# Kernel tuning notes

Measured on AMD Instinct MI355X. Metric: run time of the kernel, lower is better.

Reference implementation:

```python
import jax, jax.numpy as jnp
import numpy as np

DIM = 128
N_VAR = 100000
N_CON = 100000
N_NODES = 200000
N_EDGES = 640000


def setup_inputs() -> dict:
    key = jax.random.key(0)
    ks = jax.random.split(key, 25)
    d = DIM
    u = lambda k, s: jax.random.uniform(k, s, jnp.float32, -0.1, 0.1)
    inp = {
        "var_node_features": jax.random.normal(ks[0], (N_VAR, 2), jnp.float32),
        "con_node_features": jax.random.normal(ks[1], (N_CON, 2), jnp.float32),
        "node_types": jax.random.randint(ks[2], (N_NODES,), 0, 2),
        "assoc_var": jnp.arange(N_VAR),
        "assoc_con": N_VAR + jnp.arange(N_CON),
        "edge_index": jax.random.randint(ks[3], (2, N_EDGES), 0, N_NODES),
        "edge_types": jax.random.randint(ks[4], (N_EDGES,), 0, 2),
        "edge_features": jax.random.normal(ks[5], (N_EDGES, 1), jnp.float32),
        "var_w1": u(ks[6], (2, d)), "var_b1": u(ks[7], (d,)),
        "var_w2": u(ks[8], (d, d)), "var_b2": u(ks[9], (d,)),
        "con_w1": u(ks[10], (2, d)), "con_b1": u(ks[11], (d,)),
        "con_w2": u(ks[12], (d, d)), "con_b2": u(ks[13], (d,)),
    }
    for i, k0 in zip((1, 2, 3), (14, 17, 20)):
        inp[f"basis{i}"] = u(ks[k0], (1, d, d))      # num_bases=1
        inp[f"att{i}"] = u(ks[k0 + 1], (2, 1))       # num_relations=2
        inp[f"root{i}"] = u(ks[k0 + 2], (d, d))
        inp[f"bias{i}"] = jnp.zeros((d,), jnp.float32)
    inp["fc1_w"] = u(ks[23], (4 * d, d))
    inp["fc1_b"] = jnp.zeros((d,), jnp.float32)
    inp["fc4_w"] = u(ks[24], (d, 1))
    inp["fc4_b"] = jnp.zeros((1,), jnp.float32)
    return inp


def rgcn(x, src, dst, etype, basis, att, root, bias):
    # basis: [1, d, d], att: [2, 1] -> per-relation weights [2, d, d]
    d = x.shape[-1]
    w = (att @ basis.reshape(basis.shape[0], -1)).reshape(2, d, d)
    xj = x[src]  # [E, d] gather
    # only 2 relations: two GEMMs + select (avoids [E,d,d] materialization)
    msg = jnp.where((etype == 0)[:, None], xj @ w[0], xj @ w[1])
    s = jax.ops.segment_sum(msg, dst, num_segments=N_NODES)
    cnt = jax.ops.segment_sum(jnp.ones((dst.shape[0],), x.dtype), dst, num_segments=N_NODES)
    agg = s / jnp.maximum(cnt, 1.0)[:, None]  # mean aggregation
    return agg + x @ root + bias


def reference(var_node_features, con_node_features, node_types, assoc_var, assoc_con,
              edge_index, edge_types, edge_features,
              var_w1, var_b1, var_w2, var_b2,
              con_w1, con_b1, con_w2, con_b2,
              basis1, att1, root1, bias1,
              basis2, att2, root2, bias2,
              basis3, att3, root3, bias3,
              fc1_w, fc1_b, fc4_w, fc4_b):
    n = jnp.maximum(var_node_features @ var_w1 + var_b1, 0.0) @ var_w2 + var_b2
    e = jnp.maximum(con_node_features @ con_w1 + con_b1, 0.0) @ con_w2 + con_b2
    x = jnp.zeros((node_types.shape[0], n.shape[-1]), n.dtype)
    x = x.at[assoc_var].set(n).at[assoc_con].set(e)
    src, dst = edge_index[0], edge_index[1]
    x1 = jax.nn.relu(rgcn(x, src, dst, edge_types, basis1, att1, root1, bias1))
    x2 = jax.nn.relu(rgcn(x1, src, dst, edge_types, basis2, att2, root2, bias2))
    x3 = jax.nn.relu(rgcn(x2, src, dst, edge_types, basis3, att3, root3, bias3))
    h = jnp.concatenate([x, x1, x2, x3], axis=-1)[assoc_var]  # [n_var, 4d]
    h = jax.nn.relu(h @ fc1_w + fc1_b)
    # dropout p=0.5 is identity in eval mode
    return (h @ fc4_w + fc4_b)[:, 0]
```

## Files before the change

### kernel.cpp

```cpp
#include <hip/hip_runtime.h>
#include <hip/hip_bf16.h>

#define D 128
#define NV 100000
#define NC 100000
#define NN 200000
#define NE 640000

typedef __attribute__((ext_vector_type(4))) float f32x4;
typedef __attribute__((ext_vector_type(8))) short bf16x8;

static __device__ __forceinline__ unsigned short f2b(float f) {
    __hip_bfloat16 h = __float2bfloat16(f);
    union { __hip_bfloat16 h; unsigned short u; } c; c.h = h; return c.u;
}
static __device__ __forceinline__ float b2f(unsigned short b) {
    union { unsigned int u; float f; } c; c.u = ((unsigned int)b) << 16; return c.f;
}

template<bool RELU>
static __device__ __forceinline__ void split8v(const float f[8], bf16x8& ah, bf16x8& al)
{
    union { unsigned short s[8]; bf16x8 v; } ph, pl;
    #pragma unroll
    for (int j = 0; j < 8; ++j) {
        float x = RELU ? fmaxf(f[j], 0.f) : f[j];
        ph.s[j] = f2b(x);
        pl.s[j] = f2b(x - b2f(ph.s[j]));
    }
    ah = ph.v; al = pl.v;
}

union H8 { _Float16 h[8]; uint4 u; };
union H4 { _Float16 h[4]; uint2 u; };

struct PrepArgs { const float* src[12]; };

__global__ __launch_bounds__(256, 1) void prep_kernel(PrepArgs a, unsigned short* wt)
{
    const float* W = a.src[blockIdx.y];
    unsigned short* hi = wt + (size_t)blockIdx.y * 32768;
    unsigned short* lo = hi + 16384;
    const int o = blockIdx.x * 1024 + threadIdx.x * 4;
    const int slice = o >> 10;
    const int n     = (o >> 3) & 127;
    const int j0    = o & 7;
    union { unsigned short s[4]; unsigned long long u; } ph, pl;
    #pragma unroll
    for (int i = 0; i < 4; ++i) {
        const int k = slice * 8 + j0 + i;
        const float w = W[k * 128 + n];
        ph.s[i] = f2b(w);
        pl.s[i] = f2b(w - b2f(ph.s[i]));
    }
    *(unsigned long long*)&hi[o] = ph.u;
    *(unsigned long long*)&lo[o] = pl.u;
}

static __device__ __forceinline__ const bf16x8* wfrag(const unsigned short* wt,
                                                      int ks, int lg, int n)
{
    return (const bf16x8*)(wt + (((ks * 4 + lg) * 128) + n) * 8);
}

static __device__ __forceinline__ char* haddr(char* base, int row, int byteoff)
{
    return base + row * 256 + (byteoff ^ ((row & 7) << 4));
}

template<int AMODE, bool RELU_A>
static __device__ __forceinline__ void stage16(
    const void* A, const _Float16* agg, const float* w1, const float* b1,
    int M, int tt, int srow, int skf, int ob0, int ob1, char* hb, char* lb)
{
    int grow = tt * 32 + srow; if (grow >= M) grow = M - 1;
    float f[16];
    if (AMODE == 2) {
        const float* fr = (const float*)A + (size_t)grow * 2;
        const float f0 = fr[0], f1 = fr[1];
        #pragma unroll
        for (int q = 0; q < 4; ++q) {
            const float4 wa = *(const float4*)(w1 + skf + q * 4);
            const float4 wb = *(const float4*)(w1 + 128 + skf + q * 4);
            const float4 bb = *(const float4*)(b1 + skf + q * 4);
            f[q * 4 + 0] = fmaxf(fmaf(f0, wa.x, fmaf(f1, wb.x, bb.x)), 0.f);
            f[q * 4 + 1] = fmaxf(fmaf(f0, wa.y, fmaf(f1, wb.y, bb.y)), 0.f);
            f[q * 4 + 2] = fmaxf(fmaf(f0, wa.z, fmaf(f1, wb.z, bb.z)), 0.f);
            f[q * 4 + 3] = fmaxf(fmaf(f0, wa.w, fmaf(f1, wb.w, bb.w)), 0.f);
        }
    } else {
        const _Float16* ap = (const _Float16*)A + (size_t)grow * D + skf;
        H8 a0, a1; a0.u = ((const uint4*)ap)[0]; a1.u = ((const uint4*)ap)[1];
        #pragma unroll
        for (int j = 0; j < 8; ++j) { f[j] = (float)a0.h[j]; f[8 + j] = (float)a1.h[j]; }
        if (AMODE == 1) {
            const _Float16* gp = agg + (size_t)grow * D + skf;
            H8 g0, g1; g0.u = ((const uint4*)gp)[0]; g1.u = ((const uint4*)gp)[1];
            #pragma unroll
            for (int j = 0; j < 8; ++j) { f[j] += (float)g0.h[j]; f[8 + j] += (float)g1.h[j]; }
        }
    }
    bf16x8 h0, l0, h1, l1;
    split8v<RELU_A>(&f[0], h0, l0);
    split8v<RELU_A>(&f[8], h1, l1);
    char* hbr = hb + srow * 256;
    char* lbr = lb + srow * 256;
    *(bf16x8*)(hbr + ob0) = h0; *(bf16x8*)(hbr + ob1) = h1;
    *(bf16x8*)(lbr + ob0) = l0; *(bf16x8*)(lbr + ob1) = l1;
}

template<int AMODE, bool RELU_A, bool ADD_C>
__global__ __launch_bounds__(256, 4) void gemm5(
    const void* A, const _Float16* __restrict__ agg,
    const float* __restrict__ w1, const float* __restrict__ b1, int M,
    const unsigned short* __restrict__ wt, const float* __restrict__ bias,
    _Float16* Cout)
{
    __shared__ unsigned short Hs[2][2][32 * 128];
    const int tid  = threadIdx.x;
    const int lane = tid & 63, wv = tid >> 6;
    const int li   = lane & 15, lg = lane >> 4;
    const int colbase = wv * 32;

    bf16x8 bh[4][2], bl[4][2];
    #pragma unroll
    for (int ks = 0; ks < 4; ++ks)
        #pragma unroll
        for (int nf = 0; nf < 2; ++nf) {
            const int n = colbase + nf * 16 + li;
            bh[ks][nf] = *wfrag(wt,         ks, lg, n);
            bl[ks][nf] = *wfrag(wt + 16384, ks, lg, n);
        }

    const int ntiles = (M + 31) / 32;
    const int G = gridDim.x;
    const int t0 = blockIdx.x;
    if (t0 >= ntiles) return;

    const int srow = tid >> 3;
    const int skf  = (tid & 7) * 16;
    const int sw   = (srow & 7) << 4;
    const int ob0  = (skf * 2) ^ sw;
    const int ob1  = (skf * 2 + 16) ^ sw;

    stage16<AMODE, RELU_A>(A, agg, w1, b1, M, t0, srow, skf, ob0, ob1,
                           (char*)&Hs[0][0][0], (char*)&Hs[0][1][0]);
    __syncthreads();

    int cur = 0;
    for (int t = t0; t < ntiles; t += G) {
        const int tn = t + G;

        char* hb = (char*)&Hs[cur][0][0];
        char* lb = (char*)&Hs[cur][1][0];
        f32x4 acc[2][2];
        #pragma unroll
        for (int ms = 0; ms < 2; ++ms)
            #pragma unroll
            for (int nf = 0; nf < 2; ++nf) acc[ms][nf] = (f32x4){0.f, 0.f, 0.f, 0.f};
        #pragma unroll
        for (int ks = 0; ks < 4; ++ks) {
            const int kb = ks * 64 + lg * 16;
            bf16x8 ah[2], al[2];
            #pragma unroll
            for (int ms = 0; ms < 2; ++ms) {
                const int row = ms * 16 + li;
                ah[ms] = *(const bf16x8*)haddr(hb, row, kb);
                al[ms] = *(const bf16x8*)haddr(lb, row, kb);
            }
            #pragma unroll
            for (int nf = 0; nf < 2; ++nf)
                #pragma unroll
                for (int ms = 0; ms < 2; ++ms) {
                    acc[ms][nf] = __builtin_amdgcn_mfma_f32_16x16x32_bf16(bh[ks][nf], ah[ms], acc[ms][nf], 0, 0, 0);
                    acc[ms][nf] = __builtin_amdgcn_mfma_f32_16x16x32_bf16(bh[ks][nf], al[ms], acc[ms][nf], 0, 0, 0);
                    acc[ms][nf] = __builtin_amdgcn_mfma_f32_16x16x32_bf16(bl[ks][nf], ah[ms], acc[ms][nf], 0, 0, 0);
                }
        }

        #pragma unroll
        for (int ms = 0; ms < 2; ++ms) {
            const int grow = t * 32 + ms * 16 + li;
            if (grow < M) {
                _Float16* crow = Cout + (size_t)grow * D;
                #pragma unroll
                for (int nf = 0; nf < 2; ++nf) {
                    const int c0 = colbase + nf * 16 + lg * 4;
                    float v[4];
                    #pragma unroll
                    for (int r = 0; r < 4; ++r) v[r] = acc[ms][nf][r];
                    if (bias) {
                        const float4 b = *(const float4*)(bias + c0);
                        v[0] += b.x; v[1] += b.y; v[2] += b.z; v[3] += b.w;
                    }
                    H4 pk;
                    if (ADD_C) {
                        H4 rd; rd.u = *(const uint2*)(crow + c0);
                        #pragma unroll
                        for (int r = 0; r < 4; ++r) v[r] += (float)rd.h[r];
                    }
                    #pragma unroll
                    for (int r = 0; r < 4; ++r) pk.h[r] = (_Float16)v[r];
                    *(uint2*)(crow + c0) = pk.u;
                }
            }
        }

        if (tn < ntiles)
            stage16<AMODE, RELU_A>(A, agg, w1, b1, M, tn, srow, skf, ob0, ob1,
                                   (char*)&Hs[cur ^ 1][0][0], (char*)&Hs[cur ^ 1][1][0]);
        __syncthreads();
        cur ^= 1;
    }
}

template<bool RELU_A, bool HASAGG>
__global__ __launch_bounds__(512, 4) void layer5(
    _Float16* x, const _Float16* __restrict__ agg, int M, int Mroot,
    const unsigned short* __restrict__ wtb, const unsigned short* __restrict__ wtr,
    const float* __restrict__ bias, unsigned short* __restrict__ y)
{
    __shared__ unsigned short Hs[2][2][32 * 128];
    const int tid  = threadIdx.x;
    const int lane = tid & 63, wv = tid >> 6;
    const int li   = lane & 15, lg = lane >> 4;
    const int isroot  = wv >> 2;
    const int colbase = (wv & 3) * 32;
    const unsigned short* wsel = isroot ? wtr : wtb;

    bf16x8 bh[4][2], bl[4][2];
    #pragma unroll
    for (int ks = 0; ks < 4; ++ks)
        #pragma unroll
        for (int nf = 0; nf < 2; ++nf) {
            const int n = colbase + nf * 16 + li;
            bh[ks][nf] = *wfrag(wsel,         ks, lg, n);
            bl[ks][nf] = *wfrag(wsel + 16384, ks, lg, n);
        }
    float4 bv[2] = {{0,0,0,0},{0,0,0,0}};
    if (isroot) {
        bv[0] = *(const float4*)(bias + colbase + 0  + lg * 4);
        bv[1] = *(const float4*)(bias + colbase + 16 + lg * 4);
    }

    const int ntiles = (M + 31) / 32;
    const int G = gridDim.x;
    const int t0 = blockIdx.x;
    if (t0 >= ntiles) return;

    const int srow = tid >> 4;
    const int skf  = (tid & 15) * 8;
    const int sw   = (srow & 7) << 4;
    const int ob0  = (skf * 2) ^ sw;

    #define STAGE_L(TT, BUF)                                                     \
    {                                                                            \
        int grow = (TT) * 32 + srow; if (grow >= M) grow = M - 1;                \
        const _Float16* ap = x + (size_t)grow * D + skf;                         \
        H8 a0; a0.u = *(const uint4*)ap;                                         \
        float f[8];                                                              \
        _Pragma("unroll")                                                        \
        for (int j = 0; j < 8; ++j) f[j] = (float)a0.h[j];                       \
        if (HASAGG) {                                                            \
            H8 g0; g0.u = *(const uint4*)(agg + (size_t)grow * D + skf);         \
            _Pragma("unroll")                                                    \
            for (int j = 0; j < 8; ++j) f[j] += (float)g0.h[j];                  \
        }                                                                        \
        bf16x8 h0, l0;                                                           \
        split8v<RELU_A>(f, h0, l0);                                             \
        *(bf16x8*)((char*)&Hs[BUF][0][0] + srow * 256 + ob0) = h0;               \
        *(bf16x8*)((char*)&Hs[BUF][1][0] + srow * 256 + ob0) = l0;               \
    }

    STAGE_L(t0, 0);
    __syncthreads();

    int cur = 0;
    for (int t = t0; t < ntiles; t += G) {
        const int tn = t + G;

        char* hb = (char*)&Hs[cur][0][0];
        char* lb = (char*)&Hs[cur][1][0];
        f32x4 acc[2][2];
        #pragma unroll
        for (int ms = 0; ms < 2; ++ms)
            #pragma unroll
            for (int nf = 0; nf < 2; ++nf) acc[ms][nf] = (f32x4){0.f, 0.f, 0.f, 0.f};
        #pragma unroll
        for (int ks = 0; ks < 4; ++ks) {
            const int kb = ks * 64 + lg * 16;
            bf16x8 ah[2], al[2];
            #pragma unroll
            for (int ms = 0; ms < 2; ++ms) {
                const int row = ms * 16 + li;
                ah[ms] = *(const bf16x8*)haddr(hb, row, kb);
                al[ms] = *(const bf16x8*)haddr(lb, row, kb);
            }
            #pragma unroll
            for (int nf = 0; nf < 2; ++nf)
                #pragma unroll
                for (int ms = 0; ms < 2; ++ms) {
                    acc[ms][nf] = __builtin_amdgcn_mfma_f32_16x16x32_bf16(bh[ks][nf], ah[ms], acc[ms][nf], 0, 0, 0);
                    acc[ms][nf] = __builtin_amdgcn_mfma_f32_16x16x32_bf16(bh[ks][nf], al[ms], acc[ms][nf], 0, 0, 0);
                    acc[ms][nf] = __builtin_amdgcn_mfma_f32_16x16x32_bf16(bl[ks][nf], ah[ms], acc[ms][nf], 0, 0, 0);
                }
        }

        #pragma unroll
        for (int ms = 0; ms < 2; ++ms) {
            const int grow = t * 32 + ms * 16 + li;
            if (!isroot) {
                if (grow < M) {
                    unsigned short* yrow = y + (size_t)grow * D;
                    #pragma unroll
                    for (int nf = 0; nf < 2; ++nf) {
                        const int c0 = colbase + nf * 16 + lg * 4;
                        union { unsigned short s[4]; uint2 v; } pk;
                        #pragma unroll
                        for (int r = 0; r < 4; ++r) pk.s[r] = f2b(acc[ms][nf][r]);
                        *(uint2*)(yrow + c0) = pk.v;
                    }
                }
            } else {
                if (grow < Mroot) {
                    _Float16* xrow = x + (size_t)grow * D;
                    #pragma unroll
                    for (int nf = 0; nf < 2; ++nf) {
                        const int c0 = colbase + nf * 16 + lg * 4;
                        const float bb[4] = {bv[nf].x, bv[nf].y, bv[nf].z, bv[nf].w};
                        H4 pk;
                        #pragma unroll
                        for (int r = 0; r < 4; ++r) pk.h[r] = (_Float16)(acc[ms][nf][r] + bb[r]);
                        *(uint2*)(xrow + c0) = pk.u;
                    }
                }
            }
        }

        if (tn < ntiles) STAGE_L(tn, cur ^ 1);
        __syncthreads();
        cur ^= 1;
    }
    #undef STAGE_L
}

__global__ void hist_kernel(const int* __restrict__ dst, int* __restrict__ deg, int ne)
{
    int g = blockIdx.x * blockDim.x + threadIdx.x;
    if (g < ne) atomicAdd(&deg[dst[g]], 1);
}

__global__ __launch_bounds__(256, 1) void scan_blk(int* __restrict__ buf,
                                                   int* __restrict__ sums, int n)
{
    __shared__ int part[256];
    const int tid  = threadIdx.x;
    const int base = blockIdx.x * 1024 + tid * 4;
    int v0 = (base + 0 < n) ? buf[base + 0] : 0;
    int v1 = (base + 1 < n) ? buf[base + 1] : 0;
    int v2 = (base + 2 < n) ? buf[base + 2] : 0;
    int v3 = (base + 3 < n) ? buf[base + 3] : 0;
    const int t0 = v0, t1 = t0 + v1, t2 = t1 + v2, t3 = t2 + v3;
    part[tid] = t3;
    __syncthreads();
    #pragma unroll
    for (int off = 1; off < 256; off <<= 1) {
        int x = part[tid];
        if (tid >= off) x += part[tid - off];
        __syncthreads();
        part[tid] = x;
        __syncthreads();
    }
    if (tid == 255) sums[blockIdx.x] = part[255];
    const int excl = tid ? part[tid - 1] : 0;
    if (base + 0 < n) buf[base + 0] = excl;
    if (base + 1 < n) buf[base + 1] = excl + t0;
    if (base + 2 < n) buf[base + 2] = excl + t1;
    if (base + 3 < n) buf[base + 3] = excl + t2;
}

__global__ __launch_bounds__(256, 1) void scan_top(int* __restrict__ sums, int nb)
{
    __shared__ int part[256];
    const int tid = threadIdx.x;
    part[tid] = (tid < nb) ? sums[tid] : 0;
    __syncthreads();
    #pragma unroll
    for (int off = 1; off < 256; off <<= 1) {
        int x = part[tid];
        if (tid >= off) x += part[tid - off];
        __syncthreads();
        part[tid] = x;
        __syncthreads();
    }
    if (tid < nb) sums[tid] = tid ? part[tid - 1] : 0;
}

__global__ void scan_add(int* __restrict__ buf, const int* __restrict__ sums, int n)
{
    int i = blockIdx.x * blockDim.x + threadIdx.x;
    if (i < n) buf[i] += sums[i >> 10];
}

__global__ void fill_kernel(const int* __restrict__ src, const int* __restrict__ dst,
                            const int* __restrict__ etype,
                            int* __restrict__ cursor, int* __restrict__ edges, int ne)
{
    int e = blockIdx.x * blockDim.x + threadIdx.x;
    if (e < ne) {
        const int pos = atomicAdd(&cursor[dst[e]], 1);
        edges[pos] = (src[e] << 1) | (etype[e] & 1);
    }
}

__global__ __launch_bounds__(256, 2) void gather_agg(
    const int* __restrict__ cursor, const int* __restrict__ edges,
    const float* __restrict__ att, const unsigned short* __restrict__ y,
    _Float16* __restrict__ agg, int nn)
{
    const int gid  = blockIdx.x * 256 + threadIdx.x;
    const int node = gid >> 4;
    const int l    = gid & 15;
    if (node >= nn) return;
    const int end   = cursor[node];
    const int start = node ? cursor[node - 1] : 0;
    const float a0 = att[0], a1 = att[1];
    float s0[8] = {0,0,0,0,0,0,0,0}, s1[8] = {0,0,0,0,0,0,0,0};
    int j = start;
    for (; j + 2 <= end; j += 2) {
        const int p0 = edges[j], p1 = edges[j + 1];
        const float w0 = (p0 & 1) ? a1 : a0;
        const float w1 = (p1 & 1) ? a1 : a0;
        const uint4 va = ((const uint4*)(y + ((size_t)(p0 >> 1)) * D))[l];
        const uint4 vb = ((const uint4*)(y + ((size_t)(p1 >> 1)) * D))[l];
        const unsigned int wa[4] = {va.x, va.y, va.z, va.w};
        const unsigned int wb[4] = {vb.x, vb.y, vb.z, vb.w};
        #pragma unroll
        for (int q = 0; q < 4; ++q) {
            s0[q * 2 + 0] = fmaf(w0, b2f((unsigned short)(wa[q] & 0xFFFF)), s0[q * 2 + 0]);
            s0[q * 2 + 1] = fmaf(w0, b2f((unsigned short)(wa[q] >> 16)),    s0[q * 2 + 1]);
            s1[q * 2 + 0] = fmaf(w1, b2f((unsigned short)(wb[q] & 0xFFFF)), s1[q * 2 + 0]);
            s1[q * 2 + 1] = fmaf(w1, b2f((unsigned short)(wb[q] >> 16)),    s1[q * 2 + 1]);
        }
    }
    if (j < end) {
        const int p0 = edges[j];
        const float w0 = (p0 & 1) ? a1 : a0;
        const uint4 va = ((const uint4*)(y + ((size_t)(p0 >> 1)) * D))[l];
        const unsigned int wa[4] = {va.x, va.y, va.z, va.w};
        #pragma unroll
        for (int q = 0; q < 4; ++q) {
            s0[q * 2 + 0] = fmaf(w0, b2f((unsigned short)(wa[q] & 0xFFFF)), s0[q * 2 + 0]);
            s0[q * 2 + 1] = fmaf(w0, b2f((unsigned short)(wa[q] >> 16)),    s0[q * 2 + 1]);
        }
    }
    const float inv = 1.0f / fmaxf((float)(end - start), 1.0f);
    H8 o;
    #pragma unroll
    for (int q = 0; q < 8; ++q) o.h[q] = (_Float16)((s0[q] + s1[q]) * inv);
    *(uint4*)(agg + (size_t)node * D + l * 8) = o.u;
}

__global__ void final_kernel(
    const _Float16* __restrict__ u, const float* __restrict__ fc1_b,
    const float* __restrict__ fc4_w, const float* __restrict__ fc4_b,
    float* __restrict__ out, int n)
{
    int gid = blockIdx.x * blockDim.x + threadIdx.x;
    int row = gid >> 5, lane = gid & 31;
    if (row >= n) return;
    H4 uv; uv.u = ((const uint2*)(u + (size_t)row * D))[lane];
    float4 b = ((const float4*)fc1_b)[lane];
    float4 w = ((const float4*)fc4_w)[lane];
    float s = fmaxf((float)uv.h[0] + b.x, 0.f) * w.x
            + fmaxf((float)uv.h[1] + b.y, 0.f) * w.y
            + fmaxf((float)uv.h[2] + b.z, 0.f) * w.z
            + fmaxf((float)uv.h[3] + b.w, 0.f) * w.w;
    #pragma unroll
    for (int off = 1; off < 32; off <<= 1) s += __shfl_xor(s, off);
    if (lane == 0) out[row] = s + fc4_b[0];
}

extern "C" void kernel_launch(void* const* d_in, const int* in_sizes, int n_in,
                              void* d_out, int out_size, void* d_ws, size_t ws_size,
                              hipStream_t stream)
{
    const float* varf      = (const float*)d_in[0];
    const float* conf      = (const float*)d_in[1];
    const int*   edge_src  = (const int*)d_in[5];
    const int*   edge_dst  = edge_src + NE;
    const int*   etype     = (const int*)d_in[6];
    const float* var_w1 = (const float*)d_in[8];
    const float* var_b1 = (const float*)d_in[9];
    const float* var_w2 = (const float*)d_in[10];
    const float* var_b2 = (const float*)d_in[11];
    const float* con_w1 = (const float*)d_in[12];
    const float* con_b1 = (const float*)d_in[13];
    const float* con_w2 = (const float*)d_in[14];
    const float* con_b2 = (const float*)d_in[15];
    const float* basisL[3] = {(const float*)d_in[16], (const float*)d_in[20], (const float*)d_in[24]};
    const float* attL[3]   = {(const float*)d_in[17], (const float*)d_in[21], (const float*)d_in[25]};
    const float* rootL[3]  = {(const float*)d_in[18], (const float*)d_in[22], (const float*)d_in[26]};
    const float* biasL[3]  = {(const float*)d_in[19], (const float*)d_in[23], (const float*)d_in[27]};
    const float* fc1_w = (const float*)d_in[28];
    const float* fc1_b = (const float*)d_in[29];
    const float* fc4_w = (const float*)d_in[30];
    const float* fc4_b = (const float*)d_in[31];

    const size_t XB  = (size_t)NN * D * 2;
    const size_t YB  = (size_t)NN * D * 2;
    const size_t AB  = (size_t)NN * D * 2;
    const size_t UB  = (size_t)NV * D * 2;
    const size_t CUR = (size_t)NN * 4;
    const size_t EDG = (size_t)NE * 4;
    const size_t SUM = 4096;
    const size_t WT  = (size_t)12 * 32768 * 2;
    const size_t need = XB + YB + AB + UB + CUR + EDG + SUM + WT;
    if (ws_size < need) {
        hipMemsetAsync(d_out, 0, (size_t)out_size * sizeof(float), stream);
        return;
    }
    char* p = (char*)d_ws;
    _Float16*       x      = (_Float16*)p;       p += XB;
    unsigned short* y      = (unsigned short*)p; p += YB;
    _Float16*       agg    = (_Float16*)p;       p += AB;
    _Float16*       u      = (_Float16*)p;       p += UB;
    int*            cursor = (int*)p;            p += CUR;
    int*            edges  = (int*)p;            p += EDG;
    int*            sums   = (int*)p;            p += SUM;
    unsigned short* wt     = (unsigned short*)p;

    PrepArgs pa;
    pa.src[0] = basisL[0]; pa.src[1] = basisL[1]; pa.src[2] = basisL[2];
    pa.src[3] = rootL[0];  pa.src[4] = rootL[1];  pa.src[5] = rootL[2];
    pa.src[6] = fc1_w;                 pa.src[7] = fc1_w + 128 * 128;
    pa.src[8] = fc1_w + 2 * 128 * 128; pa.src[9] = fc1_w + 3 * 128 * 128;
    pa.src[10] = var_w2;               pa.src[11] = con_w2;
    prep_kernel<<<dim3(16, 12), 256, 0, stream>>>(pa, wt);

    hipMemsetAsync(cursor, 0, CUR, stream);
    hist_kernel<<<(NE + 255) / 256, 256, 0, stream>>>(edge_dst, cursor, NE);
    const int nblk = (NN + 1023) / 1024;
    scan_blk<<<nblk, 256, 0, stream>>>(cursor, sums, NN);
    scan_top<<<1, 256, 0, stream>>>(sums, nblk);
    scan_add<<<(NN + 255) / 256, 256, 0, stream>>>(cursor, sums, NN);
    fill_kernel<<<(NE + 255) / 256, 256, 0, stream>>>(edge_src, edge_dst, etype,
                                                      cursor, edges, NE);

    const int GM = 1024;
    const int GL = 1024;

    gemm5<2, false, false><<<GM, 256, 0, stream>>>(
        varf, nullptr, var_w1, var_b1, NV, wt + (size_t)10 * 32768, var_b2, x);
    gemm5<2, false, false><<<GM, 256, 0, stream>>>(
        conf, nullptr, con_w1, con_b1, NC, wt + (size_t)11 * 32768, con_b2,
        x + (size_t)NV * D);

    gemm5<0, false, false><<<GM, 256, 0, stream>>>(
        x, nullptr, nullptr, nullptr, NV, wt + (size_t)6 * 32768, nullptr, u);

    for (int l = 0; l < 3; ++l) {
        const unsigned short* wb_ = wt + (size_t)l * 32768;
        const unsigned short* wr_ = wt + (size_t)(3 + l) * 32768;
        const int mroot = (l == 2) ? NV : NN;
        const int gn    = (l == 2) ? NV : NN;
        if (l == 0)
            layer5<false, false><<<GL, 512, 0, stream>>>(x, nullptr, NN, mroot, wb_, wr_, biasL[0], y);
        else
            layer5<true, true><<<GL, 512, 0, stream>>>(x, agg, NN, mroot, wb_, wr_, biasL[l], y);
        gather_agg<<<(gn * 16 + 255) / 256, 256, 0, stream>>>(
            cursor, edges, attL[l], y, agg, gn);
        gemm5<1, true, true><<<GM, 256, 0, stream>>>(
            x, agg, nullptr, nullptr, NV, wt + (size_t)(7 + l) * 32768, nullptr, u);
    }

    final_kernel<<<(NV * 32 + 255) / 256, 256, 0, stream>>>(
        u, fc1_b, fc4_w, fc4_b, (float*)d_out, NV);
}
```

Before: 442.0 us.

## Fuse fc1 partial GEMMs into layer kernels and prefetch next tile into registers

Each layer kernel gets a third group of four waves, 768 threads per block, that multiplies the staged activation tile by the matching fc1 weight slice and accumulates into u. This removes the separate fc1 GEMM passes that re-read x and agg. Only the last layer's fc1 slice keeps its own GEMM. Both GEMM kernels now load the next tile's global data into registers before the MFMA loop and write it to shared memory afterwards, so load latency overlaps compute. The changes add register pressure, drop occupancy bounds to 3 blocks, and cut the layer grid to 256 blocks, which may reduce parallelism.

New measurement: 411.9 us (median of 2 runs). 1.07x faster.

```diff
diff --git a/kernel.cpp b/kernel.cpp
--- a/kernel.cpp
+++ b/kernel.cpp
@@ -68,49 +68,27 @@
     return base + row * 256 + (byteoff ^ ((row & 7) << 4));
 }
 
-template<int AMODE, bool RELU_A>
-static __device__ __forceinline__ void stage16(
-    const void* A, const _Float16* agg, const float* w1, const float* b1,
-    int M, int tt, int srow, int skf, int ob0, int ob1, char* hb, char* lb)
-{
-    int grow = tt * 32 + srow; if (grow >= M) grow = M - 1;
-    float f[16];
-    if (AMODE == 2) {
-        const float* fr = (const float*)A + (size_t)grow * 2;
-        const float f0 = fr[0], f1 = fr[1];
-        #pragma unroll
-        for (int q = 0; q < 4; ++q) {
-            const float4 wa = *(const float4*)(w1 + skf + q * 4);
-            const float4 wb = *(const float4*)(w1 + 128 + skf + q * 4);
-            const float4 bb = *(const float4*)(b1 + skf + q * 4);
-            f[q * 4 + 0] = fmaxf(fmaf(f0, wa.x, fmaf(f1, wb.x, bb.x)), 0.f);
-            f[q * 4 + 1] = fmaxf(fmaf(f0, wa.y, fmaf(f1, wb.y, bb.y)), 0.f);
-            f[q * 4 + 2] = fmaxf(fmaf(f0, wa.z, fmaf(f1, wb.z, bb.z)), 0.f);
-            f[q * 4 + 3] = fmaxf(fmaf(f0, wa.w, fmaf(f1, wb.w, bb.w)), 0.f);
-        }
-    } else {
-        const _Float16* ap = (const _Float16*)A + (size_t)grow * D + skf;
-        H8 a0, a1; a0.u = ((const uint4*)ap)[0]; a1.u = ((const uint4*)ap)[1];
-        #pragma unroll
-        for (int j = 0; j < 8; ++j) { f[j] = (float)a0.h[j]; f[8 + j] = (float)a1.h[j]; }
-        if (AMODE == 1) {
-            const _Float16* gp = agg + (size_t)grow * D + skf;
-            H8 g0, g1; g0.u = ((const uint4*)gp)[0]; g1.u = ((const uint4*)gp)[1];
-            #pragma unroll
-            for (int j = 0; j < 8; ++j) { f[j] += (float)g0.h[j]; f[8 + j] += (float)g1.h[j]; }
-        }
-    }
-    bf16x8 h0, l0, h1, l1;
-    split8v<RELU_A>(&f[0], h0, l0);
-    split8v<RELU_A>(&f[8], h1, l1);
-    char* hbr = hb + srow * 256;
-    char* lbr = lb + srow * 256;
-    *(bf16x8*)(hbr + ob0) = h0; *(bf16x8*)(hbr + ob1) = h1;
-    *(bf16x8*)(lbr + ob0) = l0; *(bf16x8*)(lbr + ob1) = l1;
+template<bool RELU, bool HASAGG>
+static __device__ __forceinline__ void wsplit8(uint4 xv, uint4 gv,
+                                               char* hb, char* lb, int srow, int ob0)
+{
+    H8 a0; a0.u = xv;
+    float f[8];
+    #pragma unroll
+    for (int j = 0; j < 8; ++j) f[j] = (float)a0.h[j];
+    if (HASAGG) {
+        H8 g0; g0.u = gv;
+        #pragma unroll
+        for (int j = 0; j < 8; ++j) f[j] += (float)g0.h[j];
+    }
+    bf16x8 h0, l0;
+    split8v<RELU>(f, h0, l0);
+    *(bf16x8*)(hb + srow * 256 + ob0) = h0;
+    *(bf16x8*)(lb + srow * 256 + ob0) = l0;
 }
 
 template<int AMODE, bool RELU_A, bool ADD_C>
-__global__ __launch_bounds__(256, 4) void gemm5(
+__global__ __launch_bounds__(256, 4) void gemm6(
     const void* A, const _Float16* __restrict__ agg,
     const float* __restrict__ w1, const float* __restrict__ b1, int M,
     const unsigned short* __restrict__ wt, const float* __restrict__ bias,
@@ -143,13 +121,64 @@
     const int ob0  = (skf * 2) ^ sw;
     const int ob1  = (skf * 2 + 16) ^ sw;
 
-    stage16<AMODE, RELU_A>(A, agg, w1, b1, M, t0, srow, skf, ob0, ob1,
-                           (char*)&Hs[0][0][0], (char*)&Hs[0][1][0]);
+    #define LOADT(TT, XV0, XV1, GV0, GV1, FV)                                    \
+    {                                                                            \
+        int grow = (TT) * 32 + srow; if (grow >= M) grow = M - 1;                \
+        if (AMODE == 2) {                                                        \
+            FV = *(const float2*)((const float*)A + (size_t)grow * 2);           \
+        } else {                                                                 \
+            const uint4* ap = (const uint4*)((const _Float16*)A + (size_t)grow * D + skf); \
+            XV0 = ap[0]; XV1 = ap[1];                                            \
+            if (AMODE == 1) {                                                    \
+                const uint4* gp = (const uint4*)(agg + (size_t)grow * D + skf);  \
+                GV0 = gp[0]; GV1 = gp[1];                                        \
+            }                                                                    \
+        }                                                                        \
+    }
+    #define WRITET(BUF, XV0, XV1, GV0, GV1, FV)                                  \
+    {                                                                            \
+        char* hb_ = (char*)&Hs[BUF][0][0];                                       \
+        char* lb_ = (char*)&Hs[BUF][1][0];                                       \
+        if (AMODE == 2) {                                                        \
+            float f[16];                                                         \
+            const float f0 = FV.x, f1 = FV.y;                                    \
+            _Pragma("unroll")                                                    \
+            for (int q = 0; q < 4; ++q) {                                        \
+                const float4 wa = *(const float4*)(w1 + skf + q * 4);            \
+                const float4 wb = *(const float4*)(w1 + 128 + skf + q * 4);      \
+                const float4 bb = *(const float4*)(b1 + skf + q * 4);            \
+                f[q*4+0] = fmaxf(fmaf(f0, wa.x, fmaf(f1, wb.x, bb.x)), 0.f);     \
+                f[q*4+1] = fmaxf(fmaf(f0, wa.y, fmaf(f1, wb.y, bb.y)), 0.f);     \
+                f[q*4+2] = fmaxf(fmaf(f0, wa.z, fmaf(f1, wb.z, bb.z)), 0.f);     \
+                f[q*4+3] = fmaxf(fmaf(f0, wa.w, fmaf(f1, wb.w, bb.w)), 0.f);     \
+            }                                                                    \
+            bf16x8 h0, l0, h1, l1;                                               \
+            split8v<RELU_A>(&f[0], h0, l0);                                     \
+            split8v<RELU_A>(&f[8], h1, l1);                                     \
+            char* hbr = hb_ + srow * 256; char* lbr = lb_ + srow * 256;          \
+            *(bf16x8*)(hbr + ob0) = h0; *(bf16x8*)(hbr + ob1) = h1;              \
+            *(bf16x8*)(lbr + ob0) = l0; *(bf16x8*)(lbr + ob1) = l1;              \
+        } else {                                                                 \
+            wsplit8<RELU_A, AMODE == 1>(XV0, GV0, hb_, lb_, srow, ob0);          \
+            wsplit8<RELU_A, AMODE == 1>(XV1, GV1, hb_, lb_, srow, ob1);          \
+        }                                                                        \
+    }
+
+    {
+        uint4 xv0 = {0,0,0,0}, xv1 = {0,0,0,0}, gv0 = {0,0,0,0}, gv1 = {0,0,0,0};
+        float2 fv = {0, 0};
+        LOADT(t0, xv0, xv1, gv0, gv1, fv);
+        WRITET(0, xv0, xv1, gv0, gv1, fv);
+    }
     __syncthreads();
 
     int cur = 0;
     for (int t = t0; t < ntiles; t += G) {
         const int tn = t + G;
+        const bool pf = tn < ntiles;
+        uint4 xv0 = {0,0,0,0}, xv1 = {0,0,0,0}, gv0 = {0,0,0,0}, gv1 = {0,0,0,0};
+        float2 fv = {0, 0};
+        if (pf) LOADT(tn, xv0, xv1, gv0, gv1, fv);
 
         char* hb = (char*)&Hs[cur][0][0];
         char* lb = (char*)&Hs[cur][1][0];
@@ -193,12 +222,12 @@
                         const float4 b = *(const float4*)(bias + c0);
                         v[0] += b.x; v[1] += b.y; v[2] += b.z; v[3] += b.w;
                     }
-                    H4 pk;
                     if (ADD_C) {
                         H4 rd; rd.u = *(const uint2*)(crow + c0);
                         #pragma unroll
                         for (int r = 0; r < 4; ++r) v[r] += (float)rd.h[r];
                     }
+                    H4 pk;
                     #pragma unroll
                     for (int r = 0; r < 4; ++r) pk.h[r] = (_Float16)v[r];
                     *(uint2*)(crow + c0) = pk.u;
@@ -206,27 +235,28 @@
             }
         }
 
-        if (tn < ntiles)
-            stage16<AMODE, RELU_A>(A, agg, w1, b1, M, tn, srow, skf, ob0, ob1,
-                                   (char*)&Hs[cur ^ 1][0][0], (char*)&Hs[cur ^ 1][1][0]);
+        if (pf) WRITET(cur ^ 1, xv0, xv1, gv0, gv1, fv);
         __syncthreads();
         cur ^= 1;
     }
-}
-
-template<bool RELU_A, bool HASAGG>
-__global__ __launch_bounds__(512, 4) void layer5(
+    #undef LOADT
+    #undef WRITET
+}
+
+template<bool RELU_A, bool HASAGG, bool UADD>
+__global__ __launch_bounds__(768, 3) void layer6(
     _Float16* x, const _Float16* __restrict__ agg, int M, int Mroot,
     const unsigned short* __restrict__ wtb, const unsigned short* __restrict__ wtr,
-    const float* __restrict__ bias, unsigned short* __restrict__ y)
+    const unsigned short* __restrict__ wtu, const float* __restrict__ bias,
+    unsigned short* __restrict__ y, _Float16* __restrict__ u, int Mu)
 {
     __shared__ unsigned short Hs[2][2][32 * 128];
     const int tid  = threadIdx.x;
     const int lane = tid & 63, wv = tid >> 6;
     const int li   = lane & 15, lg = lane >> 4;
-    const int isroot  = wv >> 2;
+    const int wgrp = wv >> 2;
     const int colbase = (wv & 3) * 32;
-    const unsigned short* wsel = isroot ? wtr : wtb;
+    const unsigned short* wsel = (wgrp == 0) ? wtb : (wgrp == 1) ? wtr : wtu;
 
     bf16x8 bh[4][2], bl[4][2];
     #pragma unroll
@@ -238,7 +268,7 @@
             bl[ks][nf] = *wfrag(wsel + 16384, ks, lg, n);
         }
     float4 bv[2] = {{0,0,0,0},{0,0,0,0}};
-    if (isroot) {
+    if (wgrp == 1) {
         bv[0] = *(const float4*)(bias + colbase + 0  + lg * 4);
         bv[1] = *(const float4*)(bias + colbase + 16 + lg * 4);
     }
@@ -248,36 +278,31 @@
     const int t0 = blockIdx.x;
     if (t0 >= ntiles) return;
 
-    const int srow = tid >> 4;
+    const bool stager = tid < 512;
+    const int srow = (tid & 511) >> 4;
     const int skf  = (tid & 15) * 8;
     const int sw   = (srow & 7) << 4;
     const int ob0  = (skf * 2) ^ sw;
 
-    #define STAGE_L(TT, BUF)                                                     \
-    {                                                                            \
-        int grow = (TT) * 32 + srow; if (grow >= M) grow = M - 1;                \
-        const _Float16* ap = x + (size_t)grow * D + skf;                         \
-        H8 a0; a0.u = *(const uint4*)ap;                                         \
-        float f[8];                                                              \
-        _Pragma("unroll")                                                        \
-        for (int j = 0; j < 8; ++j) f[j] = (float)a0.h[j];                       \
-        if (HASAGG) {                                                            \
-            H8 g0; g0.u = *(const uint4*)(agg + (size_t)grow * D + skf);         \
-            _Pragma("unroll")                                                    \
-            for (int j = 0; j < 8; ++j) f[j] += (float)g0.h[j];                  \
-        }                                                                        \
-        bf16x8 h0, l0;                                                           \
-        split8v<RELU_A>(f, h0, l0);                                             \
-        *(bf16x8*)((char*)&Hs[BUF][0][0] + srow * 256 + ob0) = h0;               \
-        *(bf16x8*)((char*)&Hs[BUF][1][0] + srow * 256 + ob0) = l0;               \
-    }
-
-    STAGE_L(t0, 0);
+    if (stager) {
+        int grow = t0 * 32 + srow; if (grow >= M) grow = M - 1;
+        uint4 xv = *(const uint4*)(x + (size_t)grow * D + skf);
+        uint4 gv = {0,0,0,0};
+        if (HASAGG) gv = *(const uint4*)(agg + (size_t)grow * D + skf);
+        wsplit8<RELU_A, HASAGG>(xv, gv, (char*)&Hs[0][0][0], (char*)&Hs[0][1][0], srow, ob0);
+    }
     __syncthreads();
 
     int cur = 0;
     for (int t = t0; t < ntiles; t += G) {
         const int tn = t + G;
+        const bool pf = stager && (tn < ntiles);
+        uint4 xv = {0,0,0,0}, gv = {0,0,0,0};
+        if (pf) {
+            int grow = tn * 32 + srow; if (grow >= M) grow = M - 1;
+            xv = *(const uint4*)(x + (size_t)grow * D + skf);
+            if (HASAGG) gv = *(const uint4*)(agg + (size_t)grow * D + skf);
+        }
 
         char* hb = (char*)&Hs[cur][0][0];
         char* lb = (char*)&Hs[cur][1][0];
@@ -309,7 +334,7 @@
         #pragma unroll
         for (int ms = 0; ms < 2; ++ms) {
             const int grow = t * 32 + ms * 16 + li;
-            if (!isroot) {
+            if (wgrp == 0) {
                 if (grow < M) {
                     unsigned short* yrow = y + (size_t)grow * D;
                     #pragma unroll
@@ -321,7 +346,7 @@
                         *(uint2*)(yrow + c0) = pk.v;
                     }
                 }
-            } else {
+            } else if (wgrp == 1) {
                 if (grow < Mroot) {
                     _Float16* xrow = x + (size_t)grow * D;
                     #pragma unroll
@@ -334,14 +359,35 @@
                         *(uint2*)(xrow + c0) = pk.u;
                     }
                 }
+            } else {
+                if (grow < Mu) {
+                    _Float16* urow = u + (size_t)grow * D;
+                    #pragma unroll
+                    for (int nf = 0; nf < 2; ++nf) {
+                        const int c0 = colbase + nf * 16 + lg * 4;
+                        float v[4];
+                        #pragma unroll
+                        for (int r = 0; r < 4; ++r) v[r] = acc[ms][nf][r];
+                        if (UADD) {
+                            H4 rd; rd.u = *(const uint2*)(urow + c0);
+                            #pragma unroll
+                            for (int r = 0; r < 4; ++r) v[r] += (float)rd.h[r];
+                        }
+                        H4 pk;
+                        #pragma unroll
+                        for (int r = 0; r < 4; ++r) pk.h[r] = (_Float16)v[r];
+                        *(uint2*)(urow + c0) = pk.u;
+                    }
+                }
             }
         }
 
-        if (tn < ntiles) STAGE_L(tn, cur ^ 1);
+        if (pf)
+            wsplit8<RELU_A, HASAGG>(xv, gv, (char*)&Hs[cur ^ 1][0][0],
+                                    (char*)&Hs[cur ^ 1][1][0], srow, ob0);
         __syncthreads();
         cur ^= 1;
     }
-    #undef STAGE_L
 }
 
 __global__ void hist_kernel(const int* __restrict__ dst, int* __restrict__ deg, int ne)
@@ -548,31 +594,32 @@
                                                       cursor, edges, NE);
 
     const int GM = 1024;
-    const int GL = 1024;
-
-    gemm5<2, false, false><<<GM, 256, 0, stream>>>(
+    const int GL = 256;
+
+    gemm6<2, false, false><<<GM, 256, 0, stream>>>(
         varf, nullptr, var_w1, var_b1, NV, wt + (size_t)10 * 32768, var_b2, x);
-    gemm5<2, false, false><<<GM, 256, 0, stream>>>(
+    gemm6<2, false, false><<<GM, 256, 0, stream>>>(
         conf, nullptr, con_w1, con_b1, NC, wt + (size_t)11 * 32768, con_b2,
         x + (size_t)NV * D);
-
-    gemm5<0, false, false><<<GM, 256, 0, stream>>>(
-        x, nullptr, nullptr, nullptr, NV, wt + (size_t)6 * 32768, nullptr, u);
 
     for (int l = 0; l < 3; ++l) {
         const unsigned short* wb_ = wt + (size_t)l * 32768;
         const unsigned short* wr_ = wt + (size_t)(3 + l) * 32768;
+        const unsigned short* wu_ = wt + (size_t)(6 + l) * 32768;
         const int mroot = (l == 2) ? NV : NN;
         const int gn    = (l == 2) ? NV : NN;
         if (l == 0)
-            layer5<false, false><<<GL, 512, 0, stream>>>(x, nullptr, NN, mroot, wb_, wr_, biasL[0], y);
+            layer6<false, false, false><<<GL, 768, 0, stream>>>(
+                x, nullptr, NN, mroot, wb_, wr_, wu_, biasL[0], y, u, NV);
         else
-            layer5<true, true><<<GL, 512, 0, stream>>>(x, agg, NN, mroot, wb_, wr_, biasL[l], y);
+            layer6<true, true, true><<<GL, 768, 0, stream>>>(
+                x, agg, NN, mroot, wb_, wr_, wu_, biasL[l], y, u, NV);
         gather_agg<<<(gn * 16 + 255) / 256, 256, 0, stream>>>(
             cursor, edges, attL[l], y, agg, gn);
-        gemm5<1, true, true><<<GM, 256, 0, stream>>>(
-            x, agg, nullptr, nullptr, NV, wt + (size_t)(7 + l) * 32768, nullptr, u);
-    }
+    }
+
+    gemm6<1, true, true><<<GM, 256, 0, stream>>>(
+        x, agg, nullptr, nullptr, NV, wt + (size_t)9 * 32768, nullptr, u);
 
     final_kernel<<<(NV * 32 + 255) / 256, 256, 0, stream>>>(
         u, fc1_b, fc4_w, fc4_b, (float*)d_out, NV);
```
